# Kernel optimization log

Hardware: AMD Instinct MI355X
Metric: run time of the kernel (lower is better)

## Reference

```python
import jax, jax.numpy as jnp
import numpy as np
import math

H, DK, D = 8, 64, 512  # heads, head dim, d_model

def _layernorm(x, g, b, eps=1e-6):
    # Matches custom LayerNorm: unbiased std (torch.std default), divide by (std+eps)
    mean = x.mean(-1, keepdims=True)
    std = jnp.sqrt(((x - mean) ** 2).sum(-1, keepdims=True) / (x.shape[-1] - 1))
    return g * (x - mean) / (std + eps) + b

def _mha(q, k, v, Wq, bq, Wk, bk, Wv, bv, Wo, bo, mask=None, know=False):
    B = q.shape[0]
    split = lambda x, W, b: (x @ W + b).reshape(B, -1, H, DK).transpose(0, 2, 1, 3)
    qh, kh, vh = split(q, Wq, bq), split(k, Wk, bk), split(v, Wv, bv)
    s = jnp.einsum('bhqd,bhkd->bhqk', qh, kh) / math.sqrt(DK)
    if mask is not None:
        m = mask[:, None]  # [B,1,Nq,Nk] broadcast over heads
        if know:
            s = s * m  # attention_know multiplies scores by mask first
        s = jnp.where(m == 0, -1e9, s)
    p = jax.nn.softmax(s, axis=-1)
    o = jnp.einsum('bhqk,bhkd->bhqd', p, vh).transpose(0, 2, 1, 3).reshape(B, -1, H * DK)
    return o @ Wo + bo

def setup_inputs() -> dict:
    key = jax.random.key(0)
    ks = iter(jax.random.split(key, 64))
    p = lambda *shape: jax.random.normal(next(ks), shape, jnp.float32) * 0.02
    B = 512
    inp = {
        'visual_inputs': jax.random.normal(next(ks), (B, 24, 2048), jnp.float32),
        'entity_inputs': jax.random.normal(next(ks), (B, 33, 4096), jnp.float32),
        'pathological_graph': jax.random.uniform(next(ks), (B, 33, 33), dtype=jnp.float32),
        'vis_W': p(2048, 512), 'vis_b': jnp.zeros(512, jnp.float32),
        'ent_W': p(4096, 512), 'ent_b': jnp.zeros(512, jnp.float32),
        'ca_Wq': p(512, 512), 'ca_bq': jnp.zeros(512, jnp.float32),
        'ca_Wk': p(512, 512), 'ca_bk': jnp.zeros(512, jnp.float32),
        'ca_Wv': p(512, 512), 'ca_bv': jnp.zeros(512, jnp.float32),
        'ca_Wo': p(512, 512), 'ca_bo': jnp.zeros(512, jnp.float32),
        'kp_W': p(512, 512), 'kp_b': jnp.zeros(512, jnp.float32),
        'pred_W': p(33 * 33, 33 * 33), 'pred_b': jnp.zeros(33 * 33, jnp.float32),
        'l_Wq': p(3, 512, 512), 'l_bq': jnp.zeros((3, 512), jnp.float32),
        'l_Wk': p(3, 512, 512), 'l_bk': jnp.zeros((3, 512), jnp.float32),
        'l_Wv': p(3, 512, 512), 'l_bv': jnp.zeros((3, 512), jnp.float32),
        'l_Wo': p(3, 512, 512), 'l_bo': jnp.zeros((3, 512), jnp.float32),
        'l_ffW1': p(3, 512, 512), 'l_ffb1': jnp.zeros((3, 512), jnp.float32),
        'l_ffW2': p(3, 512, 512), 'l_ffb2': jnp.zeros((3, 512), jnp.float32),
        'l_n1_g': jnp.ones((3, 512), jnp.float32), 'l_n1_b': jnp.zeros((3, 512), jnp.float32),
        'l_n2_g': jnp.ones((3, 512), jnp.float32), 'l_n2_b': jnp.zeros((3, 512), jnp.float32),
        'fin_g': jnp.ones(512, jnp.float32), 'fin_b': jnp.zeros(512, jnp.float32),
        'ad_W1': p(512, 512), 'ad_b1': jnp.zeros(512, jnp.float32),
        'ad_W2': p(512, 4096), 'ad_b2': jnp.zeros(4096, jnp.float32),
        'sc_fc_W': p(512, 128), 'sc_fc_b': jnp.zeros(128, jnp.float32),
        'sc_cls_W': p(33 * 128, 32), 'sc_cls_b': jnp.zeros(32, jnp.float32),
    }
    return inp

def reference(visual_inputs, entity_inputs, pathological_graph,
              vis_W, vis_b, ent_W, ent_b,
              ca_Wq, ca_bq, ca_Wk, ca_bk, ca_Wv, ca_bv, ca_Wo, ca_bo,
              kp_W, kp_b, pred_W, pred_b,
              l_Wq, l_bq, l_Wk, l_bk, l_Wv, l_bv, l_Wo, l_bo,
              l_ffW1, l_ffb1, l_ffW2, l_ffb2,
              l_n1_g, l_n1_b, l_n2_g, l_n2_b,
              fin_g, fin_b,
              ad_W1, ad_b1, ad_W2, ad_b2,
              sc_fc_W, sc_fc_b, sc_cls_W, sc_cls_b):
    B = visual_inputs.shape[0]
    v = visual_inputs @ vis_W + vis_b   # [B,24,512]
    e = entity_inputs @ ent_W + ent_b   # [B,33,512]
    # Cross attention: entities attend to visual tokens (no mask)
    ef = _mha(e, v, v, ca_Wq, ca_bq, ca_Wk, ca_bk, ca_Wv, ca_bv, ca_Wo, ca_bo)
    er = ef @ kp_W + kp_b
    rel = jnp.einsum('bnd,bmd->bnm', er, er)  # [B,33,33]
    emp = jax.nn.sigmoid(rel.reshape(B, -1) @ pred_W + pred_b).reshape(B, 33, 33)
    adj = 0.9 * pathological_graph + 0.1 * emp
    # Grapher: 3 layers; note sublayer norms the query but K/V are the un-normed x
    x = ef
    for i in range(3):
        xn = _layernorm(x, l_n1_g[i], l_n1_b[i])
        att = _mha(xn, x, x, l_Wq[i], l_bq[i], l_Wk[i], l_bk[i], l_Wv[i], l_bv[i],
                   l_Wo[i], l_bo[i], mask=adj, know=True)
        x = x + att
        xn2 = _layernorm(x, l_n2_g[i], l_n2_b[i])
        ff = jax.nn.relu(xn2 @ l_ffW1[i] + l_ffb1[i]) @ l_ffW2[i] + l_ffb2[i]
        x = x + ff
    emb = _layernorm(x, fin_g, fin_b)  # [B,33,512]
    adapted = (emb @ ad_W1 + ad_b1) @ ad_W2 + ad_b2  # [B,33,4096]
    cls_in = (emb @ sc_fc_W + sc_fc_b).reshape(B, -1)  # [B,33*128]
    cls_res = jax.nn.sigmoid(cls_in @ sc_cls_W + sc_cls_b)  # [B,32]
    return (adapted, cls_res)
```

## Files before the change

### kernel.cpp

```cpp
#include <hip/hip_runtime.h>
#include <hip/hip_bf16.h>
#include <math.h>


typedef unsigned short ushort_t;
typedef short short8 __attribute__((ext_vector_type(8)));
typedef float floatx4 __attribute__((ext_vector_type(4)));

__device__ __forceinline__ unsigned short f2u(float f) {
    union { float f; unsigned u; } x; x.f = f;
    unsigned r = x.u + 0x7fffu + ((x.u >> 16) & 1u);
    return (unsigned short)(r >> 16);
}
__device__ __forceinline__ float u2f(unsigned short u) {
    union { unsigned u; float f; } x; x.u = ((unsigned)u) << 16; return x.f;
}

struct WJob { const float* src; ushort_t* dst; int K; int N; int Kd; int block0; };
struct WJobs { WJob j[29]; int n; };

__global__ __launch_bounds__(256) void wcvt_k(WJobs jb)
{
    const int bid = blockIdx.x, tid = threadIdx.x;
    int ji = 0;
    for (int t = 1; t < jb.n; ++t) if (jb.j[t].block0 <= bid) ji = t;
    const WJob w = jb.j[ji];
    const int lb = bid - w.block0;
    const int tilesN = (w.N + 31) >> 5;
    const int tk = lb / tilesN, tn = lb - tk * tilesN;
    const int k0 = tk * 32, n0 = tn * 32;
    __shared__ float T[32][33];
    const int c = tid & 31, rr = tid >> 5;
#pragma unroll
    for (int p = 0; p < 4; ++p) {
        int r = rr + p * 8;
        int k = k0 + r, n = n0 + c;
        T[r][c] = (k < w.K && n < w.N) ? w.src[(size_t)k * w.N + n] : 0.f;
    }
    __syncthreads();
#pragma unroll
    for (int p = 0; p < 4; ++p) {
        int r = rr + p * 8;
        int n = n0 + r, k = k0 + c;
        if (n < w.N && k < w.Kd) w.dst[(size_t)n * w.Kd + k] = f2u(T[c][r]);
    }
}

template<int EPI, bool AF32, bool WB, bool WF>
__global__ __launch_bounds__(256) void mfma_gemm(
    const void* __restrict__ Av, int lda,
    const ushort_t* __restrict__ Bt, int ldb,
    const float* __restrict__ bias,
    const float* __restrict__ res,
    float* __restrict__ Cf, ushort_t* __restrict__ Cb,
    int M, int N, int K)
{
    __shared__ __align__(16) ushort_t As[128][72];
    __shared__ __align__(16) ushort_t Bs[128][72];

    const int tid  = threadIdx.x;
    const int lane = tid & 63, wave = tid >> 6;
    const int wr = (wave >> 1) * 64, wc = (wave & 1) * 64;
    const int lrow = lane & 15, quad = lane >> 4;
    const int row0 = blockIdx.y * 128, col0 = blockIdx.x * 128;

    const int srow  = tid >> 3;
    const int skoff = (tid & 7) * 8;

    floatx4 acc[4][4];
#pragma unroll
    for (int i = 0; i < 4; ++i)
#pragma unroll
        for (int j = 0; j < 4; ++j) acc[i][j] = (floatx4){0.f, 0.f, 0.f, 0.f};

    for (int k0 = 0; k0 < K; k0 += 64) {
#pragma unroll
        for (int p = 0; p < 4; ++p) {
            const int r = p * 32 + srow;
            uint4 val;
            if (AF32) {
                const float* pa = (const float*)Av + (size_t)(row0 + r) * lda + k0 + skoff;
                float4 f0 = *(const float4*)pa;
                float4 f1 = *(const float4*)(pa + 4);
                val.x = (unsigned)f2u(f0.x) | ((unsigned)f2u(f0.y) << 16);
                val.y = (unsigned)f2u(f0.z) | ((unsigned)f2u(f0.w) << 16);
                val.z = (unsigned)f2u(f1.x) | ((unsigned)f2u(f1.y) << 16);
                val.w = (unsigned)f2u(f1.z) | ((unsigned)f2u(f1.w) << 16);
            } else {
                val = *(const uint4*)((const ushort_t*)Av + (size_t)(row0 + r) * lda + k0 + skoff);
            }
            *(uint4*)&As[r][skoff] = val;
        }
#pragma unroll
        for (int p = 0; p < 4; ++p) {
            const int r = p * 32 + srow;
            const int n = col0 + r;
            uint4 val = make_uint4(0u, 0u, 0u, 0u);
            if (n < N) val = *(const uint4*)(Bt + (size_t)n * ldb + k0 + skoff);
            *(uint4*)&Bs[r][skoff] = val;
        }
        __syncthreads();

#pragma unroll
        for (int kk = 0; kk < 2; ++kk) {
            short8 af[4], bfr[4];
#pragma unroll
            for (int i = 0; i < 4; ++i)
                af[i] = *(const short8*)&As[wr + i * 16 + lrow][kk * 32 + quad * 8];
#pragma unroll
            for (int j = 0; j < 4; ++j)
                bfr[j] = *(const short8*)&Bs[wc + j * 16 + lrow][kk * 32 + quad * 8];
#pragma unroll
            for (int i = 0; i < 4; ++i)
#pragma unroll
                for (int j = 0; j < 4; ++j)
                    acc[i][j] = __builtin_amdgcn_mfma_f32_16x16x32_bf16(af[i], bfr[j], acc[i][j], 0, 0, 0);
        }
        __syncthreads();
    }

#pragma unroll
    for (int j = 0; j < 4; ++j) {
        const int col = col0 + wc + j * 16 + lrow;
        if (col >= N) continue;
        const float bv = bias[col];
#pragma unroll
        for (int i = 0; i < 4; ++i) {
#pragma unroll
            for (int r = 0; r < 4; ++r) {
                const int row = row0 + wr + i * 16 + quad * 4 + r;
                const size_t off = (size_t)row * N + col;
                float v = acc[i][j][r] + bv;
                if (EPI == 1) v = fmaxf(v, 0.f);
                if (EPI == 2) v += res[off];
                if (EPI == 4) v = 0.9f * res[off] + 0.1f * (1.f / (1.f + __expf(-v)));
                if (WF) Cf[off] = v;
                if (WB) Cb[off] = f2u(v);
            }
        }
    }
}

__global__ __launch_bounds__(256) void ln_k(
    const float* __restrict__ x, const float* __restrict__ g,
    const float* __restrict__ b, ushort_t* __restrict__ out)
{
    const int row = blockIdx.x;
    const int tid = threadIdx.x;
    const float* xr = x + (size_t)row * 512;
    float v0 = xr[tid], v1 = xr[tid + 256];

    __shared__ float red[4];
    float s = v0 + v1;
#pragma unroll
    for (int off = 32; off >= 1; off >>= 1) s += __shfl_down(s, off);
    if ((tid & 63) == 0) red[tid >> 6] = s;
    __syncthreads();
    const float mean = (red[0] + red[1] + red[2] + red[3]) * (1.f / 512.f);
    const float d0 = v0 - mean, d1 = v1 - mean;
    __syncthreads();

    float ss = d0 * d0 + d1 * d1;
#pragma unroll
    for (int off = 32; off >= 1; off >>= 1) ss += __shfl_down(ss, off);
    if ((tid & 63) == 0) red[tid >> 6] = ss;
    __syncthreads();
    const float var = (red[0] + red[1] + red[2] + red[3]) * (1.f / 511.f);
    const float inv = 1.f / (sqrtf(var) + 1e-6f);

    ushort_t* orow = out + (size_t)row * 512;
    orow[tid]       = f2u(g[tid]       * (d0 * inv) + b[tid]);
    orow[tid + 256] = f2u(g[tid + 256] * (d1 * inv) + b[tid + 256]);
}

__global__ __launch_bounds__(256) void cross_attn_k(
    const ushort_t* __restrict__ q, const ushort_t* __restrict__ k,
    const ushort_t* __restrict__ v, ushort_t* __restrict__ out)
{
    const int h = blockIdx.x, b = blockIdx.y, tid = threadIdx.x;
    __shared__ float Lq[33 * 64], Lk[24 * 64], Lv[24 * 64], Ls[33 * 24];
    const size_t qoff = ((size_t)b * 33) * 512 + h * 64;
    const size_t koff = ((size_t)b * 24) * 512 + h * 64;

    for (int i = tid; i < 33 * 64; i += 256) {
        int t = i >> 6, d = i & 63;
        Lq[i] = u2f(q[qoff + (size_t)t * 512 + d]);
    }
    for (int i = tid; i < 24 * 64; i += 256) {
        int t = i >> 6, d = i & 63;
        Lk[i] = u2f(k[koff + (size_t)t * 512 + d]);
        Lv[i] = u2f(v[koff + (size_t)t * 512 + d]);
    }
    __syncthreads();

    for (int i = tid; i < 33 * 24; i += 256) {
        int r = i / 24, c = i % 24;
        float s = 0.f;
#pragma unroll
        for (int d = 0; d < 64; ++d) s = fmaf(Lq[r * 64 + d], Lk[c * 64 + d], s);
        Ls[i] = s * 0.125f;
    }
    __syncthreads();

    if (tid < 33) {
        float mx = -1e30f;
        for (int c = 0; c < 24; ++c) mx = fmaxf(mx, Ls[tid * 24 + c]);
        float sum = 0.f;
        for (int c = 0; c < 24; ++c) { float e = __expf(Ls[tid * 24 + c] - mx); Ls[tid * 24 + c] = e; sum += e; }
        float inv = 1.f / sum;
        for (int c = 0; c < 24; ++c) Ls[tid * 24 + c] *= inv;
    }
    __syncthreads();

    for (int i = tid; i < 33 * 64; i += 256) {
        int r = i >> 6, d = i & 63;
        float a = 0.f;
#pragma unroll
        for (int c = 0; c < 24; ++c) a = fmaf(Ls[r * 24 + c], Lv[c * 64 + d], a);
        out[qoff + (size_t)r * 512 + d] = f2u(a);
    }
}

__global__ __launch_bounds__(256) void self_attn_k(
    const ushort_t* __restrict__ q, const ushort_t* __restrict__ k,
    const ushort_t* __restrict__ v, const float* __restrict__ adj,
    ushort_t* __restrict__ out)
{
    const int h = blockIdx.x, b = blockIdx.y, tid = threadIdx.x;
    __shared__ float Lq[33 * 64], Lk[33 * 64], Lv[33 * 64], Ls[33 * 34], Lm[33 * 33];
    const size_t off = ((size_t)b * 33) * 512 + h * 64;

    for (int i = tid; i < 33 * 64; i += 256) {
        int t = i >> 6, d = i & 63;
        Lq[i] = u2f(q[off + (size_t)t * 512 + d]);
        Lk[i] = u2f(k[off + (size_t)t * 512 + d]);
        Lv[i] = u2f(v[off + (size_t)t * 512 + d]);
    }
    for (int i = tid; i < 1089; i += 256) Lm[i] = adj[(size_t)b * 1089 + i];
    __syncthreads();

    for (int i = tid; i < 1089; i += 256) {
        int r = i / 33, c = i % 33;
        float s = 0.f;
#pragma unroll
        for (int d = 0; d < 64; ++d) s = fmaf(Lq[r * 64 + d], Lk[c * 64 + d], s);
        s *= 0.125f;
        float m = Lm[i];
        s = (m == 0.f) ? -1e9f : s * m;
        Ls[r * 34 + c] = s;
    }
    __syncthreads();

    if (tid < 33) {
        float mx = -1e30f;
        for (int c = 0; c < 33; ++c) mx = fmaxf(mx, Ls[tid * 34 + c]);
        float sum = 0.f;
        for (int c = 0; c < 33; ++c) { float e = __expf(Ls[tid * 34 + c] - mx); Ls[tid * 34 + c] = e; sum += e; }
        float inv = 1.f / sum;
        for (int c = 0; c < 33; ++c) Ls[tid * 34 + c] *= inv;
    }
    __syncthreads();

    for (int i = tid; i < 33 * 64; i += 256) {
        int r = i >> 6, d = i & 63;
        float a = 0.f;
#pragma unroll
        for (int c = 0; c < 33; ++c) a = fmaf(Ls[r * 34 + c], Lv[c * 64 + d], a);
        out[off + (size_t)r * 512 + d] = f2u(a);
    }
}

__global__ __launch_bounds__(256) void rel_k(
    const ushort_t* __restrict__ er, ushort_t* __restrict__ rel)
{
    const int b = blockIdx.x, tid = threadIdx.x;
    __shared__ float E[33 * 256];
    const ushort_t* src = er + (size_t)b * 33 * 512;

    float accv[5] = {0.f, 0.f, 0.f, 0.f, 0.f};
    for (int half = 0; half < 2; ++half) {
        for (int i = tid; i < 33 * 256; i += 256) {
            int t = i >> 8, d = i & 255;
            E[i] = u2f(src[(size_t)t * 512 + half * 256 + d]);
        }
        __syncthreads();
        for (int u = 0; u < 5; ++u) {
            int i = tid + 256 * u;
            if (i < 1089) {
                int r = i / 33, c = i % 33;
                const float* pr = &E[r * 256];
                const float* pc = &E[c * 256];
                float a = accv[u];
                for (int d = 0; d < 256; d += 4) {
                    float4 x = *(const float4*)&pr[d];
                    float4 y = *(const float4*)&pc[d];
                    a = fmaf(x.x, y.x, fmaf(x.y, y.y, fmaf(x.z, y.z, fmaf(x.w, y.w, a))));
                }
                accv[u] = a;
            }
        }
        __syncthreads();
    }
    for (int u = 0; u < 5; ++u) {
        int i = tid + 256 * u;
        if (i < 1089) rel[(size_t)b * 1152 + i] = f2u(accv[u]);
    }
    for (int i = 1089 + tid; i < 1152; i += 256) rel[(size_t)b * 1152 + i] = 0;
}

__global__ __launch_bounds__(256) void cls_k(
    const ushort_t* __restrict__ cin, const float* __restrict__ W,
    const float* __restrict__ bias, float* __restrict__ out)
{
    const int b = blockIdx.x, tid = threadIdx.x;
    const int n = tid & 31, kg = tid >> 5;
    const ushort_t* x = cin + (size_t)b * 4224;
    float acc = 0.f;
    for (int k = kg; k < 4224; k += 8)
        acc = fmaf(u2f(x[k]), W[(size_t)k * 32 + n], acc);

    __shared__ float part[8][32];
    part[kg][n] = acc;
    __syncthreads();
    if (tid < 32) {
        float s = bias[tid];
#pragma unroll
        for (int g = 0; g < 8; ++g) s += part[g][tid];
        out[(size_t)b * 32 + tid] = 1.f / (1.f + __expf(-s));
    }
}

extern "C" void kernel_launch(void* const* d_in, const int* in_sizes, int n_in,
                              void* d_out, int out_size, void* d_ws, size_t ws_size,
                              hipStream_t stream)
{
    const float* visual   = (const float*)d_in[0];
    const float* entity   = (const float*)d_in[1];
    const float* graph    = (const float*)d_in[2];
    const float* vis_W    = (const float*)d_in[3];
    const float* vis_b    = (const float*)d_in[4];
    const float* ent_W    = (const float*)d_in[5];
    const float* ent_b    = (const float*)d_in[6];
    const float* ca_Wq    = (const float*)d_in[7];
    const float* ca_bq    = (const float*)d_in[8];
    const float* ca_Wk    = (const float*)d_in[9];
    const float* ca_bk    = (const float*)d_in[10];
    const float* ca_Wv    = (const float*)d_in[11];
    const float* ca_bv    = (const float*)d_in[12];
    const float* ca_Wo    = (const float*)d_in[13];
    const float* ca_bo    = (const float*)d_in[14];
    const float* kp_W     = (const float*)d_in[15];
    const float* kp_b     = (const float*)d_in[16];
    const float* pred_W   = (const float*)d_in[17];
    const float* pred_b   = (const float*)d_in[18];
    const float* l_Wq     = (const float*)d_in[19];
    const float* l_bq     = (const float*)d_in[20];
    const float* l_Wk     = (const float*)d_in[21];
    const float* l_bk     = (const float*)d_in[22];
    const float* l_Wv     = (const float*)d_in[23];
    const float* l_bv     = (const float*)d_in[24];
    const float* l_Wo     = (const float*)d_in[25];
    const float* l_bo     = (const float*)d_in[26];
    const float* l_ffW1   = (const float*)d_in[27];
    const float* l_ffb1   = (const float*)d_in[28];
    const float* l_ffW2   = (const float*)d_in[29];
    const float* l_ffb2   = (const float*)d_in[30];
    const float* l_n1_g   = (const float*)d_in[31];
    const float* l_n1_b   = (const float*)d_in[32];
    const float* l_n2_g   = (const float*)d_in[33];
    const float* l_n2_b   = (const float*)d_in[34];
    const float* fin_g    = (const float*)d_in[35];
    const float* fin_b    = (const float*)d_in[36];
    const float* ad_W1    = (const float*)d_in[37];
    const float* ad_b1    = (const float*)d_in[38];
    const float* ad_W2    = (const float*)d_in[39];
    const float* ad_b2    = (const float*)d_in[40];
    const float* sc_fc_W  = (const float*)d_in[41];
    const float* sc_fc_b  = (const float*)d_in[42];
    const float* sc_cls_W = (const float*)d_in[43];
    const float* sc_cls_b = (const float*)d_in[44];

    const int B  = 512;
    const int Mv = B * 24;
    const int Me = B * 33;

    char* wsb = (char*)d_ws;
    size_t off = 0;
    auto alloc_us = [&](size_t elems) -> ushort_t* {
        ushort_t* p = (ushort_t*)(wsb + off); off += ((elems * 2 + 255) & ~(size_t)255); return p; };
    auto alloc_f = [&](size_t elems) -> float* {
        float* p = (float*)(wsb + off); off += ((elems * 4 + 255) & ~(size_t)255); return p; };

    ushort_t* vis_Wt = alloc_us((size_t)512 * 2048);
    ushort_t* ent_Wt = alloc_us((size_t)512 * 4096);
    ushort_t* caq_t  = alloc_us((size_t)512 * 512);
    ushort_t* cak_t  = alloc_us((size_t)512 * 512);
    ushort_t* cav_t  = alloc_us((size_t)512 * 512);
    ushort_t* cao_t  = alloc_us((size_t)512 * 512);
    ushort_t* kp_t   = alloc_us((size_t)512 * 512);
    ushort_t* pred_t = alloc_us((size_t)1089 * 1152);
    ushort_t* lw_t   = alloc_us((size_t)18 * 512 * 512);
    ushort_t* ad1_t  = alloc_us((size_t)512 * 512);
    ushort_t* ad2_t  = alloc_us((size_t)4096 * 512);
    ushort_t* fc_t   = alloc_us((size_t)128 * 512);

    float* o_x   = alloc_f((size_t)Me * 512);
    float* o_adj = alloc_f((size_t)B * 1089);

    ushort_t* o_xb  = alloc_us((size_t)Me * 512);
    ushort_t* o_xn  = alloc_us((size_t)Me * 512);
    ushort_t* o_q   = alloc_us((size_t)Me * 512);
    ushort_t* o_k   = alloc_us((size_t)Me * 512);
    ushort_t* o_vv  = alloc_us((size_t)Me * 512);
    ushort_t* o_v   = alloc_us((size_t)Mv * 512);
    ushort_t* o_rel = alloc_us((size_t)B * 1152);
    ushort_t* o_cls = alloc_us((size_t)Me * 128);

    float* out_adapted = (float*)d_out;
    float* out_cls     = out_adapted + (size_t)Me * 4096;

    WJobs J; int nb = 0, ji = 0;
    auto addjob = [&](const float* src, ushort_t* dst, int K, int N, int Kd) {
        J.j[ji].src = src; J.j[ji].dst = dst; J.j[ji].K = K; J.j[ji].N = N;
        J.j[ji].Kd = Kd; J.j[ji].block0 = nb;
        nb += ((Kd + 31) / 32) * ((N + 31) / 32);
        ++ji;
    };
    addjob(vis_W, vis_Wt, 2048, 512, 2048);
    addjob(ent_W, ent_Wt, 4096, 512, 4096);
    addjob(ca_Wq, caq_t, 512, 512, 512);
    addjob(ca_Wk, cak_t, 512, 512, 512);
    addjob(ca_Wv, cav_t, 512, 512, 512);
    addjob(ca_Wo, cao_t, 512, 512, 512);
    addjob(kp_W,  kp_t,  512, 512, 512);
    addjob(pred_W, pred_t, 1089, 1089, 1152);
    for (int i = 0; i < 3; ++i) {
        addjob(l_Wq   + (size_t)i * 262144, lw_t + (size_t)(i * 6 + 0) * 262144, 512, 512, 512);
        addjob(l_Wk   + (size_t)i * 262144, lw_t + (size_t)(i * 6 + 1) * 262144, 512, 512, 512);
        addjob(l_Wv   + (size_t)i * 262144, lw_t + (size_t)(i * 6 + 2) * 262144, 512, 512, 512);
        addjob(l_Wo   + (size_t)i * 262144, lw_t + (size_t)(i * 6 + 3) * 262144, 512, 512, 512);
        addjob(l_ffW1 + (size_t)i * 262144, lw_t + (size_t)(i * 6 + 4) * 262144, 512, 512, 512);
        addjob(l_ffW2 + (size_t)i * 262144, lw_t + (size_t)(i * 6 + 5) * 262144, 512, 512, 512);
    }
    addjob(ad_W1, ad1_t, 512, 512, 512);
    addjob(ad_W2, ad2_t, 512, 4096, 512);
    addjob(sc_fc_W, fc_t, 512, 128, 512);
    J.n = ji;

    dim3 blk(256);
    wcvt_k<<<dim3(nb), blk, 0, stream>>>(J);

    auto g2 = [](int M, int N) { return dim3((unsigned)((N + 127) / 128), (unsigned)(M / 128)); };
    dim3 attn_grid(8, B);

    mfma_gemm<0, true, true, false><<<g2(Mv, 512), blk, 0, stream>>>(
        visual, 2048, vis_Wt, 2048, vis_b, nullptr, nullptr, o_v, Mv, 512, 2048);
    mfma_gemm<0, true, true, false><<<g2(Me, 512), blk, 0, stream>>>(
        entity, 4096, ent_Wt, 4096, ent_b, nullptr, nullptr, o_xn, Me, 512, 4096);

    mfma_gemm<0, false, true, false><<<g2(Me, 512), blk, 0, stream>>>(
        o_xn, 512, caq_t, 512, ca_bq, nullptr, nullptr, o_q, Me, 512, 512);
    mfma_gemm<0, false, true, false><<<g2(Mv, 512), blk, 0, stream>>>(
        o_v, 512, cak_t, 512, ca_bk, nullptr, nullptr, o_k, Mv, 512, 512);
    mfma_gemm<0, false, true, false><<<g2(Mv, 512), blk, 0, stream>>>(
        o_v, 512, cav_t, 512, ca_bv, nullptr, nullptr, o_vv, Mv, 512, 512);
    cross_attn_k<<<attn_grid, blk, 0, stream>>>(o_q, o_k, o_vv, o_xn);
    mfma_gemm<0, false, true, true><<<g2(Me, 512), blk, 0, stream>>>(
        o_xn, 512, cao_t, 512, ca_bo, nullptr, o_x, o_xb, Me, 512, 512);

    mfma_gemm<0, false, true, false><<<g2(Me, 512), blk, 0, stream>>>(
        o_xb, 512, kp_t, 512, kp_b, nullptr, nullptr, o_q, Me, 512, 512);
    rel_k<<<dim3(B), blk, 0, stream>>>(o_q, o_rel);
    mfma_gemm<4, false, false, true><<<g2(512, 1089), blk, 0, stream>>>(
        o_rel, 1152, pred_t, 1152, pred_b, graph, o_adj, nullptr, 512, 1089, 1152);

    for (int i = 0; i < 3; ++i) {
        const ushort_t* Wq = lw_t + (size_t)(i * 6 + 0) * 262144;
        const ushort_t* Wk = lw_t + (size_t)(i * 6 + 1) * 262144;
        const ushort_t* Wv = lw_t + (size_t)(i * 6 + 2) * 262144;
        const ushort_t* Wo = lw_t + (size_t)(i * 6 + 3) * 262144;
        const ushort_t* W1 = lw_t + (size_t)(i * 6 + 4) * 262144;
        const ushort_t* W2 = lw_t + (size_t)(i * 6 + 5) * 262144;

        ln_k<<<dim3(Me), blk, 0, stream>>>(o_x, l_n1_g + (size_t)i * 512, l_n1_b + (size_t)i * 512, o_xn);
        mfma_gemm<0, false, true, false><<<g2(Me, 512), blk, 0, stream>>>(
            o_xn, 512, Wq, 512, l_bq + (size_t)i * 512, nullptr, nullptr, o_q, Me, 512, 512);
        mfma_gemm<0, false, true, false><<<g2(Me, 512), blk, 0, stream>>>(
            o_xb, 512, Wk, 512, l_bk + (size_t)i * 512, nullptr, nullptr, o_k, Me, 512, 512);
        mfma_gemm<0, false, true, false><<<g2(Me, 512), blk, 0, stream>>>(
            o_xb, 512, Wv, 512, l_bv + (size_t)i * 512, nullptr, nullptr, o_vv, Me, 512, 512);
        self_attn_k<<<attn_grid, blk, 0, stream>>>(o_q, o_k, o_vv, o_adj, o_xn);
        mfma_gemm<2, false, true, true><<<g2(Me, 512), blk, 0, stream>>>(
            o_xn, 512, Wo, 512, l_bo + (size_t)i * 512, o_x, o_x, o_xb, Me, 512, 512);
        ln_k<<<dim3(Me), blk, 0, stream>>>(o_x, l_n2_g + (size_t)i * 512, l_n2_b + (size_t)i * 512, o_xn);
        mfma_gemm<1, false, true, false><<<g2(Me, 512), blk, 0, stream>>>(
            o_xn, 512, W1, 512, l_ffb1 + (size_t)i * 512, nullptr, nullptr, o_q, Me, 512, 512);
        mfma_gemm<2, false, true, true><<<g2(Me, 512), blk, 0, stream>>>(
            o_q, 512, W2, 512, l_ffb2 + (size_t)i * 512, o_x, o_x, o_xb, Me, 512, 512);
    }

    ln_k<<<dim3(Me), blk, 0, stream>>>(o_x, fin_g, fin_b, o_xn);
    mfma_gemm<0, false, true, false><<<g2(Me, 512), blk, 0, stream>>>(
        o_xn, 512, ad1_t, 512, ad_b1, nullptr, nullptr, o_q, Me, 512, 512);
    mfma_gemm<0, false, false, true><<<g2(Me, 4096), blk, 0, stream>>>(
        o_q, 512, ad2_t, 512, ad_b2, nullptr, out_adapted, nullptr, Me, 4096, 512);
    mfma_gemm<0, false, true, false><<<g2(Me, 128), blk, 0, stream>>>(
        o_xn, 512, fc_t, 512, sc_fc_b, nullptr, nullptr, o_cls, Me, 128, 512);
    cls_k<<<dim3(B), blk, 0, stream>>>(o_cls, sc_cls_W, sc_cls_b, out_cls);
}
```

Measured before the change: 3.403 ms.

## Add wide 64x512-tile MFMA GEMM and route N=512 GEMMs through it

Adds a GEMM kernel in which each block computes a 64-row by 512-column tile, so every A row panel is read from global memory only once per output row. It replaces the 128x128 GEMM for all N=512 and the N=4096 projections, with the aim of cutting redundant A reads, including the fp32-to-bf16 conversion of the large visual and entity inputs. In exchange the grid is much smaller (for example, 264 blocks for the entity GEMM), accumulator register use is high (128 floats per thread), and there is only a simple register double-buffer with a 32-wide K step. That may lower occupancy and latency hiding.

Result: slower. 5.871 ms (+72.5%).

```diff
diff --git a/kernel.cpp b/kernel.cpp
--- a/kernel.cpp
+++ b/kernel.cpp
@@ -43,6 +43,115 @@
         int r = rr + p * 8;
         int n = n0 + r, k = k0 + c;
         if (n < w.N && k < w.Kd) w.dst[(size_t)n * w.Kd + k] = f2u(T[c][r]);
+    }
+}
+
+template<int EPI, bool AF32, bool WB, bool WF>
+__global__ __launch_bounds__(256) void mfma_gemm_w(
+    const void* __restrict__ Av, int lda,
+    const ushort_t* __restrict__ Bt, int ldb,
+    const float* __restrict__ bias,
+    const float* __restrict__ res,
+    float* __restrict__ Cf, ushort_t* __restrict__ Cb,
+    int M, int N, int K)
+{
+    __shared__ __align__(16) ushort_t As[64][40];
+    __shared__ __align__(16) ushort_t Bs[512][40];
+
+    const int tid  = threadIdx.x;
+    const int lane = tid & 63, wave = tid >> 6;
+    const int wc = wave * 128;
+    const int lrow = lane & 15, quad = lane >> 4;
+    const int row0 = blockIdx.y * 64, col0 = blockIdx.x * 512;
+
+    const int arow = tid >> 2;
+    const int ako  = (tid & 3) * 8;
+
+    floatx4 acc[4][8];
+#pragma unroll
+    for (int i = 0; i < 4; ++i)
+#pragma unroll
+        for (int j = 0; j < 8; ++j) acc[i][j] = (floatx4){0.f, 0.f, 0.f, 0.f};
+
+    uint4 ra;
+    uint4 rb[8];
+
+    auto loadA = [&](int k0) {
+        if (AF32) {
+            const float* pa = (const float*)Av + (size_t)(row0 + arow) * lda + k0 + ako;
+            float4 f0 = *(const float4*)pa;
+            float4 f1 = *(const float4*)(pa + 4);
+            ra.x = (unsigned)f2u(f0.x) | ((unsigned)f2u(f0.y) << 16);
+            ra.y = (unsigned)f2u(f0.z) | ((unsigned)f2u(f0.w) << 16);
+            ra.z = (unsigned)f2u(f1.x) | ((unsigned)f2u(f1.y) << 16);
+            ra.w = (unsigned)f2u(f1.z) | ((unsigned)f2u(f1.w) << 16);
+        } else {
+            ra = *(const uint4*)((const ushort_t*)Av + (size_t)(row0 + arow) * lda + k0 + ako);
+        }
+    };
+    auto loadB = [&](int k0) {
+#pragma unroll
+        for (int p = 0; p < 8; ++p) {
+            const int idx = p * 256 + tid;
+            const int n = idx >> 2, ko = (idx & 3) * 8;
+            rb[p] = *(const uint4*)(Bt + (size_t)(col0 + n) * ldb + k0 + ko);
+        }
+    };
+    auto writeLDS = [&]() {
+        *(uint4*)&As[arow][ako] = ra;
+#pragma unroll
+        for (int p = 0; p < 8; ++p) {
+            const int idx = p * 256 + tid;
+            const int n = idx >> 2, ko = (idx & 3) * 8;
+            *(uint4*)&Bs[n][ko] = rb[p];
+        }
+    };
+
+    loadA(0); loadB(0);
+    writeLDS();
+    __syncthreads();
+
+    for (int k0 = 0; k0 < K; k0 += 32) {
+        const int kn = k0 + 32;
+        const bool more = (kn < K);
+        if (more) { loadA(kn); loadB(kn); }
+
+        short8 af[4], bf[8];
+#pragma unroll
+        for (int i = 0; i < 4; ++i)
+            af[i] = *(const short8*)&As[i * 16 + lrow][quad * 8];
+#pragma unroll
+        for (int j = 0; j < 8; ++j)
+            bf[j] = *(const short8*)&Bs[wc + j * 16 + lrow][quad * 8];
+#pragma unroll
+        for (int i = 0; i < 4; ++i)
+#pragma unroll
+            for (int j = 0; j < 8; ++j)
+                acc[i][j] = __builtin_amdgcn_mfma_f32_16x16x32_bf16(af[i], bf[j], acc[i][j], 0, 0, 0);
+
+        __syncthreads();
+        if (more) { writeLDS(); __syncthreads(); }
+    }
+
+#pragma unroll
+    for (int j = 0; j < 8; ++j) {
+        const int col = col0 + wc + j * 16 + lrow;
+        if (col >= N) continue;
+        const float bv = bias[col];
+#pragma unroll
+        for (int i = 0; i < 4; ++i) {
+#pragma unroll
+            for (int r = 0; r < 4; ++r) {
+                const int row = row0 + i * 16 + quad * 4 + r;
+                const size_t off = (size_t)row * N + col;
+                float v = acc[i][j][r] + bv;
+                if (EPI == 1) v = fmaxf(v, 0.f);
+                if (EPI == 2) v += res[off];
+                if (EPI == 4) v = 0.9f * res[off] + 0.1f * (1.f / (1.f + __expf(-v)));
+                if (WF) Cf[off] = v;
+                if (WB) Cb[off] = f2u(v);
+            }
+        }
     }
 }
 
@@ -450,25 +559,26 @@
     dim3 blk(256);
     wcvt_k<<<dim3(nb), blk, 0, stream>>>(J);
 
-    auto g2 = [](int M, int N) { return dim3((unsigned)((N + 127) / 128), (unsigned)(M / 128)); };
+    auto g2  = [](int M, int N) { return dim3((unsigned)((N + 127) / 128), (unsigned)(M / 128)); };
+    auto g2w = [](int M, int N) { return dim3((unsigned)(N / 512), (unsigned)(M / 64)); };
     dim3 attn_grid(8, B);
 
-    mfma_gemm<0, true, true, false><<<g2(Mv, 512), blk, 0, stream>>>(
+    mfma_gemm_w<0, true, true, false><<<g2w(Mv, 512), blk, 0, stream>>>(
         visual, 2048, vis_Wt, 2048, vis_b, nullptr, nullptr, o_v, Mv, 512, 2048);
-    mfma_gemm<0, true, true, false><<<g2(Me, 512), blk, 0, stream>>>(
+    mfma_gemm_w<0, true, true, false><<<g2w(Me, 512), blk, 0, stream>>>(
         entity, 4096, ent_Wt, 4096, ent_b, nullptr, nullptr, o_xn, Me, 512, 4096);
 
-    mfma_gemm<0, false, true, false><<<g2(Me, 512), blk, 0, stream>>>(
+    mfma_gemm_w<0, false, true, false><<<g2w(Me, 512), blk, 0, stream>>>(
         o_xn, 512, caq_t, 512, ca_bq, nullptr, nullptr, o_q, Me, 512, 512);
-    mfma_gemm<0, false, true, false><<<g2(Mv, 512), blk, 0, stream>>>(
+    mfma_gemm_w<0, false, true, false><<<g2w(Mv, 512), blk, 0, stream>>>(
         o_v, 512, cak_t, 512, ca_bk, nullptr, nullptr, o_k, Mv, 512, 512);
-    mfma_gemm<0, false, true, false><<<g2(Mv, 512), blk, 0, stream>>>(
+    mfma_gemm_w<0, false, true, false><<<g2w(Mv, 512), blk, 0, stream>>>(
         o_v, 512, cav_t, 512, ca_bv, nullptr, nullptr, o_vv, Mv, 512, 512);
     cross_attn_k<<<attn_grid, blk, 0, stream>>>(o_q, o_k, o_vv, o_xn);
-    mfma_gemm<0, false, true, true><<<g2(Me, 512), blk, 0, stream>>>(
+    mfma_gemm_w<0, false, true, true><<<g2w(Me, 512), blk, 0, stream>>>(
         o_xn, 512, cao_t, 512, ca_bo, nullptr, o_x, o_xb, Me, 512, 512);
 
-    mfma_gemm<0, false, true, false><<<g2(Me, 512), blk, 0, stream>>>(
+    mfma_gemm_w<0, false, true, false><<<g2w(Me, 512), blk, 0, stream>>>(
         o_xb, 512, kp_t, 512, kp_b, nullptr, nullptr, o_q, Me, 512, 512);
     rel_k<<<dim3(B), blk, 0, stream>>>(o_q, o_rel);
     mfma_gemm<4, false, false, true><<<g2(512, 1089), blk, 0, stream>>>(
@@ -483,26 +593,26 @@
         const ushort_t* W2 = lw_t + (size_t)(i * 6 + 5) * 262144;
 
         ln_k<<<dim3(Me), blk, 0, stream>>>(o_x, l_n1_g + (size_t)i * 512, l_n1_b + (size_t)i * 512, o_xn);
-        mfma_gemm<0, false, true, false><<<g2(Me, 512), blk, 0, stream>>>(
+        mfma_gemm_w<0, false, true, false><<<g2w(Me, 512), blk, 0, stream>>>(
             o_xn, 512, Wq, 512, l_bq + (size_t)i * 512, nullptr, nullptr, o_q, Me, 512, 512);
-        mfma_gemm<0, false, true, false><<<g2(Me, 512), blk, 0, stream>>>(
+        mfma_gemm_w<0, false, true, false><<<g2w(Me, 512), blk, 0, stream>>>(
             o_xb, 512, Wk, 512, l_bk + (size_t)i * 512, nullptr, nullptr, o_k, Me, 512, 512);
-        mfma_gemm<0, false, true, false><<<g2(Me, 512), blk, 0, stream>>>(
+        mfma_gemm_w<0, false, true, false><<<g2w(Me, 512), blk, 0, stream>>>(
             o_xb, 512, Wv, 512, l_bv + (size_t)i * 512, nullptr, nullptr, o_vv, Me, 512, 512);
         self_attn_k<<<attn_grid, blk, 0, stream>>>(o_q, o_k, o_vv, o_adj, o_xn);
-        mfma_gemm<2, false, true, true><<<g2(Me, 512), blk, 0, stream>>>(
+        mfma_gemm_w<2, false, true, true><<<g2w(Me, 512), blk, 0, stream>>>(
             o_xn, 512, Wo, 512, l_bo + (size_t)i * 512, o_x, o_x, o_xb, Me, 512, 512);
         ln_k<<<dim3(Me), blk, 0, stream>>>(o_x, l_n2_g + (size_t)i * 512, l_n2_b + (size_t)i * 512, o_xn);
-        mfma_gemm<1, false, true, false><<<g2(Me, 512), blk, 0, stream>>>(
+        mfma_gemm_w<1, false, true, false><<<g2w(Me, 512), blk, 0, stream>>>(
             o_xn, 512, W1, 512, l_ffb1 + (size_t)i * 512, nullptr, nullptr, o_q, Me, 512, 512);
-        mfma_gemm<2, false, true, true><<<g2(Me, 512), blk, 0, stream>>>(
+        mfma_gemm_w<2, false, true, true><<<g2w(Me, 512), blk, 0, stream>>>(
             o_q, 512, W2, 512, l_ffb2 + (size_t)i * 512, o_x, o_x, o_xb, Me, 512, 512);
     }
 
     ln_k<<<dim3(Me), blk, 0, stream>>>(o_x, fin_g, fin_b, o_xn);
-    mfma_gemm<0, false, true, false><<<g2(Me, 512), blk, 0, stream>>>(
+    mfma_gemm_w<0, false, true, false><<<g2w(Me, 512), blk, 0, stream>>>(
         o_xn, 512, ad1_t, 512, ad_b1, nullptr, nullptr, o_q, Me, 512, 512);
-    mfma_gemm<0, false, false, true><<<g2(Me, 4096), blk, 0, stream>>>(
+    mfma_gemm_w<0, false, false, true><<<g2w(Me, 4096), blk, 0, stream>>>(
         o_q, 512, ad2_t, 512, ad_b2, nullptr, out_adapted, nullptr, Me, 4096, 512);
     mfma_gemm<0, false, true, false><<<g2(Me, 128), blk, 0, stream>>>(
         o_xn, 512, fc_t, 512, sc_fc_b, nullptr, nullptr, o_cls, Me, 128, 512);
```
